# Kernel optimization log

Hardware: AMD Instinct MI355X
Metric: run time of the kernel (lower is better)

## Reference

```python
import jax, jax.numpy as jnp
import numpy as np


def setup_inputs() -> dict:
    key = jax.random.key(0)
    ks = jax.random.split(key, 5)
    B, T, I, H, O = 64, 1024, 128, 256, 128
    stdv = 1.0 / np.sqrt(H)
    return {
        "x": jax.random.normal(ks[0], (B, T, I), dtype=jnp.float32),
        "W": jax.random.uniform(ks[1], (I, 4 * H), dtype=jnp.float32, minval=-stdv, maxval=stdv),
        "U": jax.random.uniform(ks[2], (H, 4 * H), dtype=jnp.float32, minval=-stdv, maxval=stdv),
        "bias": jax.random.uniform(ks[3], (4 * H,), dtype=jnp.float32, minval=-stdv, maxval=stdv),
        "dense_w": jax.random.uniform(ks[4], (O, H), dtype=jnp.float32, minval=-stdv, maxval=stdv),
        "dense_b": jnp.zeros((O,), dtype=jnp.float32),
    }


def reference(x, W, U, bias, dense_w, dense_b):
    B, T, I = x.shape
    H = U.shape[0]
    # Precompute input contribution for all timesteps in one big GEMM.
    xW = jnp.einsum("bti,ig->btg", x, W) + bias  # (B, T, 4H)

    def step(carry, xw_t):
        h, c = carry
        gates = xw_t + h @ U  # (B, 4H)
        i_t = jax.nn.sigmoid(gates[:, :H])
        f_t = jax.nn.sigmoid(gates[:, H:2 * H])
        g_t = jnp.tanh(gates[:, 2 * H:3 * H])
        o_t = jax.nn.sigmoid(gates[:, 3 * H:])
        c = f_t * c + i_t * g_t
        h = o_t * jnp.tanh(c)
        return (h, c), h

    h0 = jnp.zeros((B, H), dtype=x.dtype)
    c0 = jnp.zeros((B, H), dtype=x.dtype)
    (h_T, _), _ = jax.lax.scan(step, (h0, c0), jnp.swapaxes(xW, 0, 1))
    # Original takes hidden_seq[:, -1, :] == final h_t, then Linear, then unsqueeze(2).
    out = h_T @ dense_w.T + dense_b  # (B, O)
    return out[:, :, None]  # (B, O, 1)
```

## Files before the change

kernel.cpp:

```cpp
#include <hip/hip_runtime.h>
#include <math.h>

#define TT 1024
#define BB 64
#define II 128
#define HH 256
#define OO 128
#define GPB 16
#define NCOL 64
#define Z_STRIDE 392
#define PART_BG_STRIDE 68
#define PART_RC_STRIDE 273

#define WS_HBUF_F 8192
#define WS_CLEAR_B 20480

__device__ __forceinline__ float rcp(float v) { return __builtin_amdgcn_rcpf(v); }
__device__ __forceinline__ float sigm(float v) { return rcp(1.f + __expf(-v)); }
__device__ __forceinline__ float ftanh(float v) {
    return __builtin_fmaf(-2.f, rcp(__expf(2.f * v) + 1.f), 1.f);
}

extern "C" __global__ void __launch_bounds__(256, 1) lstm_scan(
    const float* __restrict__ x, const float* __restrict__ W,
    const float* __restrict__ U, const float* __restrict__ bias,
    float* __restrict__ wsf)
{
    __shared__ float z[4 * Z_STRIDE];
    __shared__ float part[16 * PART_RC_STRIDE];
    __shared__ int   misc[8];

    int*   flags  = (int*)wsf;
    int*   abortp = ((int*)wsf) + 4096;
    float* hbuf   = wsf + WS_HBUF_F;

    const int tid  = threadIdx.x;
    const int gid  = blockIdx.x & 15;
    const int p    = blockIdx.x >> 4;
    const int cg   = tid & 15;
    const int rc   = tid >> 4;
    const int lane = tid & 63;
    const int w    = tid >> 6;
    const int myb  = 4 * gid + w;

    float wr[6][4][4];
    {
        const int c0 = cg * 4;
        const int gcol = (c0 >> 4) * HH + p * 16 + (c0 & 15);
#pragma unroll
        for (int rr = 0; rr < 6; ++rr) {
#pragma unroll
            for (int i = 0; i < 4; ++i) {
                const int r = rr * 64 + rc * 4 + i;
                const float4 wv = (rr < 2)
                    ? *(const float4*)(W + (size_t)r * 1024 + gcol)
                    : *(const float4*)(U + (size_t)(r - II) * 1024 + gcol);
                wr[rr][i][0] = wv.x; wr[rr][i][1] = wv.y;
                wr[rr][i][2] = wv.z; wr[rr][i][3] = wv.w;
            }
        }
    }
    const float bia_reg = bias[(lane >> 4) * HH + p * 16 + (lane & 15)];
    float creg = 0.f;

    for (int idx = tid; idx < 4 * Z_STRIDE; idx += 256) z[idx] = 0.f;
    if (tid < 8) misc[tid] = 0;

    if (tid < 128) {
        const int b2 = tid >> 5, l2 = tid & 31;
        const float4 xv = *(const float4*)(
            x + ((size_t)(4 * gid + b2) * TT + 0) * II + 4 * l2);
        *(float4*)(z + b2 * Z_STRIDE + 4 * l2) = xv;
    }
    __syncthreads();

    for (int t = 1; t <= TT; ++t) {
        float acc[4][4];
#pragma unroll
        for (int a = 0; a < 4; ++a)
#pragma unroll
            for (int b = 0; b < 4; ++b) acc[a][b] = 0.f;

#pragma unroll
        for (int rr = 0; rr < 2; ++rr) {
#pragma unroll
            for (int bg = 0; bg < 4; ++bg) {
                const float4 zv = *(const float4*)(z + bg * Z_STRIDE + rr * 64 + rc * 4);
#pragma unroll
                for (int c = 0; c < 4; ++c)
                    acc[bg][c] += zv.x * wr[rr][0][c] + zv.y * wr[rr][1][c]
                                + zv.z * wr[rr][2][c] + zv.w * wr[rr][3][c];
            }
        }

        if (t > 1) {
            const int need = t - 1;
            const int* fp = &flags[((lane & 15) * GPB + gid) * 16 + w * 4];
            int it = 0;
            for (;;) {
                int f1 = need, f2 = need;
                if (lane < GPB) {
                    f1 = __hip_atomic_load(fp, __ATOMIC_RELAXED, __HIP_MEMORY_SCOPE_AGENT);
                    f2 = __hip_atomic_load(fp, __ATOMIC_RELAXED, __HIP_MEMORY_SCOPE_AGENT);
                }
                if (__ballot(f1 >= need) == ~0ULL) break;
                if (__ballot(f2 >= need) == ~0ULL) break;
                if ((++it & 63) == 0) {
                    int abv = __hip_atomic_load(abortp, __ATOMIC_RELAXED,
                                                __HIP_MEMORY_SCOPE_AGENT);
                    if (abv) { if (lane == 0) misc[w] = 1; break; }
                    if (it > (1 << 19)) {
                        if (lane == 0) {
                            __hip_atomic_store(abortp, 1, __ATOMIC_RELAXED,
                                               __HIP_MEMORY_SCOPE_AGENT);
                            misc[w] = 1;
                        }
                        break;
                    }
                }
            }
            const float* hsrc = hbuf + ((size_t)((t - 1) & 1) * BB + myb) * HH;
            const float v0 = __hip_atomic_load(hsrc + lane,       __ATOMIC_RELAXED, __HIP_MEMORY_SCOPE_AGENT);
            const float v1 = __hip_atomic_load(hsrc + lane + 64,  __ATOMIC_RELAXED, __HIP_MEMORY_SCOPE_AGENT);
            const float v2 = __hip_atomic_load(hsrc + lane + 128, __ATOMIC_RELAXED, __HIP_MEMORY_SCOPE_AGENT);
            const float v3 = __hip_atomic_load(hsrc + lane + 192, __ATOMIC_RELAXED, __HIP_MEMORY_SCOPE_AGENT);
            float* zdst = z + w * Z_STRIDE + II + lane;
            zdst[0]   = v0;
            zdst[64]  = v1;
            zdst[128] = v2;
            zdst[192] = v3;
        }
        __syncthreads();
        if (misc[0] | misc[1] | misc[2] | misc[3]) break;

#pragma unroll
        for (int rr = 2; rr < 6; ++rr) {
#pragma unroll
            for (int bg = 0; bg < 4; ++bg) {
                const float4 zv = *(const float4*)(z + bg * Z_STRIDE + rr * 64 + rc * 4);
#pragma unroll
                for (int c = 0; c < 4; ++c)
                    acc[bg][c] += zv.x * wr[rr][0][c] + zv.y * wr[rr][1][c]
                                + zv.z * wr[rr][2][c] + zv.w * wr[rr][3][c];
            }
        }

#pragma unroll
        for (int bg = 0; bg < 4; ++bg)
#pragma unroll
            for (int c = 0; c < 4; ++c)
                part[rc * PART_RC_STRIDE + bg * PART_BG_STRIDE + cg * 4 + c] = acc[bg][c];
        __syncthreads();

        float s = bia_reg;
#pragma unroll
        for (int r2 = 0; r2 < 16; ++r2)
            s += part[r2 * PART_RC_STRIDE + w * PART_BG_STRIDE + lane];

        const int j = lane & 15;
        const float sf = __shfl(s, j + 16);
        const float sg = __shfl(s, j + 32);
        const float so = __shfl(s, j + 48);
        if (lane < 16) {
            const float iv = sigm(s);
            const float fv = sigm(sf);
            const float gv = ftanh(sg);
            const float ov = sigm(so);
            creg = fv * creg + iv * gv;
            const float hv = ov * ftanh(creg);
            __hip_atomic_store(
                hbuf + ((size_t)(t & 1) * BB + myb) * HH + p * 16 + j,
                hv, __ATOMIC_RELAXED, __HIP_MEMORY_SCOPE_AGENT);
        }
        asm volatile("s_waitcnt vmcnt(0)" ::: "memory");
        if (lane == 0)
            __hip_atomic_store(&flags[blockIdx.x * 16 + w * 4], t,
                               __ATOMIC_RELAXED, __HIP_MEMORY_SCOPE_AGENT);

        if (t < TT && lane >= 16 && lane < 48) {
            const int l2 = lane - 16;
            const float4 xv = *(const float4*)(
                x + ((size_t)myb * TT + t) * II + 4 * l2);
            *(float4*)(z + w * Z_STRIDE + 4 * l2) = xv;
        }
        __syncthreads();
    }
}

extern "C" __global__ void __launch_bounds__(256) lstm_out(
    const float* __restrict__ wsf, const float* __restrict__ dw,
    const float* __restrict__ db, float* __restrict__ out)
{
    __shared__ float hs[256];
    __shared__ float red[256];
    const int b = blockIdx.x;
    const int tid = threadIdx.x;
    const float* h0 = wsf + WS_HBUF_F;
    hs[tid] = h0[(size_t)b * HH + tid];
    __syncthreads();
    const int o = tid & 127, half = tid >> 7;
    const float* wrow = dw + o * HH + half * 128;
    const float* hrow = hs + half * 128;
    float s = 0.f;
#pragma unroll
    for (int k = 0; k < 128; k += 4) {
        const float4 wv = *(const float4*)(wrow + k);
        s += hrow[k] * wv.x + hrow[k + 1] * wv.y + hrow[k + 2] * wv.z + hrow[k + 3] * wv.w;
    }
    red[tid] = s;
    __syncthreads();
    if (tid < 128)
        out[(size_t)b * OO + tid] = red[tid] + red[128 + tid] + db[tid];
}

extern "C" void kernel_launch(void* const* d_in, const int* in_sizes, int n_in,
                              void* d_out, int out_size, void* d_ws, size_t ws_size,
                              hipStream_t stream)
{
    const float* x    = (const float*)d_in[0];
    const float* W    = (const float*)d_in[1];
    const float* U    = (const float*)d_in[2];
    const float* bias = (const float*)d_in[3];
    const float* dw   = (const float*)d_in[4];
    const float* db   = (const float*)d_in[5];
    float* out = (float*)d_out;
    float* ws  = (float*)d_ws;

    hipMemsetAsync(d_ws, 0, WS_CLEAR_B, stream);
    hipLaunchKernelGGL(lstm_scan, dim3(256), dim3(256), 0, stream,
                       x, W, U, bias, ws);
    hipLaunchKernelGGL(lstm_out, dim3(64), dim3(256), 0, stream, ws, dw, db, out);
}
```

Before: 2.483 ms.

## Give each wave its own batch row, removing block barriers and LDS reduction

Each wavefront now owns one batch row and computes all 64 of the block's gate columns over the full K=384 reduction, holding 96 float4 weight registers per lane. This removes the cross-thread partial-sum buffer in LDS and every __syncthreads in the time loop, so the waves synchronise only through the global flags. The next timestep's x row is prefetched into registers before the spin-wait. The cost is a 4x longer serial dot product per lane with heavy register pressure (384 weight VGPRs), plus LDS broadcast reads of z.

```diff
diff --git a/kernel.cpp b/kernel.cpp
--- a/kernel.cpp
+++ b/kernel.cpp
@@ -7,10 +7,7 @@
 #define HH 256
 #define OO 128
 #define GPB 16
-#define NCOL 64
-#define Z_STRIDE 392
-#define PART_BG_STRIDE 68
-#define PART_RC_STRIDE 273
+#define ZPAD 400
 
 #define WS_HBUF_F 8192
 #define WS_CLEAR_B 20480
@@ -26,9 +23,7 @@
     const float* __restrict__ U, const float* __restrict__ bias,
     float* __restrict__ wsf)
 {
-    __shared__ float z[4 * Z_STRIDE];
-    __shared__ float part[16 * PART_RC_STRIDE];
-    __shared__ int   misc[8];
+    __shared__ float z[4 * ZPAD];
 
     int*   flags  = (int*)wsf;
     int*   abortp = ((int*)wsf) + 4096;
@@ -37,61 +32,48 @@
     const int tid  = threadIdx.x;
     const int gid  = blockIdx.x & 15;
     const int p    = blockIdx.x >> 4;
-    const int cg   = tid & 15;
-    const int rc   = tid >> 4;
     const int lane = tid & 63;
     const int w    = tid >> 6;
     const int myb  = 4 * gid + w;
+    const int j    = lane & 15;
 
-    float wr[6][4][4];
-    {
-        const int c0 = cg * 4;
-        const int gcol = (c0 >> 4) * HH + p * 16 + (c0 & 15);
+    const int gcol = (lane >> 4) * HH + p * 16 + j;
+
+    float4 wr[96];
 #pragma unroll
-        for (int rr = 0; rr < 6; ++rr) {
-#pragma unroll
-            for (int i = 0; i < 4; ++i) {
-                const int r = rr * 64 + rc * 4 + i;
-                const float4 wv = (rr < 2)
-                    ? *(const float4*)(W + (size_t)r * 1024 + gcol)
-                    : *(const float4*)(U + (size_t)(r - II) * 1024 + gcol);
-                wr[rr][i][0] = wv.x; wr[rr][i][1] = wv.y;
-                wr[rr][i][2] = wv.z; wr[rr][i][3] = wv.w;
-            }
-        }
+    for (int k = 0; k < 96; ++k) {
+        const float* base = (k < 32)
+            ? (W + (size_t)(4 * k) * 1024 + gcol)
+            : (U + (size_t)(4 * k - 128) * 1024 + gcol);
+        wr[k].x = base[0];
+        wr[k].y = base[1024];
+        wr[k].z = base[2048];
+        wr[k].w = base[3072];
     }
-    const float bia_reg = bias[(lane >> 4) * HH + p * 16 + (lane & 15)];
+    const float bia_reg = bias[gcol];
     float creg = 0.f;
 
-    for (int idx = tid; idx < 4 * Z_STRIDE; idx += 256) z[idx] = 0.f;
-    if (tid < 8) misc[tid] = 0;
+    float* zw = z + w * ZPAD;
+    for (int i = lane; i < HH; i += 64) zw[II + i] = 0.f;
+    float4 xv = make_float4(0.f, 0.f, 0.f, 0.f);
+    if (lane < 32) {
+        xv = *(const float4*)(x + (size_t)myb * TT * II + 4 * lane);
+        *(float4*)(zw + 4 * lane) = xv;
+    }
 
-    if (tid < 128) {
-        const int b2 = tid >> 5, l2 = tid & 31;
-        const float4 xv = *(const float4*)(
-            x + ((size_t)(4 * gid + b2) * TT + 0) * II + 4 * l2);
-        *(float4*)(z + b2 * Z_STRIDE + 4 * l2) = xv;
-    }
-    __syncthreads();
-
+    int ab = 0;
     for (int t = 1; t <= TT; ++t) {
-        float acc[4][4];
-#pragma unroll
-        for (int a = 0; a < 4; ++a)
-#pragma unroll
-            for (int b = 0; b < 4; ++b) acc[a][b] = 0.f;
+        float acc[4] = {0.f, 0.f, 0.f, 0.f};
 
 #pragma unroll
-        for (int rr = 0; rr < 2; ++rr) {
-#pragma unroll
-            for (int bg = 0; bg < 4; ++bg) {
-                const float4 zv = *(const float4*)(z + bg * Z_STRIDE + rr * 64 + rc * 4);
-#pragma unroll
-                for (int c = 0; c < 4; ++c)
-                    acc[bg][c] += zv.x * wr[rr][0][c] + zv.y * wr[rr][1][c]
-                                + zv.z * wr[rr][2][c] + zv.w * wr[rr][3][c];
-            }
+        for (int k = 0; k < 32; ++k) {
+            const float4 zv = *(const float4*)(zw + 4 * k);
+            acc[k & 3] += zv.x * wr[k].x + zv.y * wr[k].y
+                        + zv.z * wr[k].z + zv.w * wr[k].w;
         }
+
+        if (t < TT && lane < 32)
+            xv = *(const float4*)(x + ((size_t)myb * TT + t) * II + 4 * lane);
 
         if (t > 1) {
             const int need = t - 1;
@@ -108,56 +90,35 @@
                 if ((++it & 63) == 0) {
                     int abv = __hip_atomic_load(abortp, __ATOMIC_RELAXED,
                                                 __HIP_MEMORY_SCOPE_AGENT);
-                    if (abv) { if (lane == 0) misc[w] = 1; break; }
+                    if (abv) { ab = 1; break; }
                     if (it > (1 << 19)) {
-                        if (lane == 0) {
+                        if (lane == 0)
                             __hip_atomic_store(abortp, 1, __ATOMIC_RELAXED,
                                                __HIP_MEMORY_SCOPE_AGENT);
-                            misc[w] = 1;
-                        }
-                        break;
+                        ab = 1; break;
                     }
                 }
             }
+            if (ab) break;
             const float* hsrc = hbuf + ((size_t)((t - 1) & 1) * BB + myb) * HH;
             const float v0 = __hip_atomic_load(hsrc + lane,       __ATOMIC_RELAXED, __HIP_MEMORY_SCOPE_AGENT);
             const float v1 = __hip_atomic_load(hsrc + lane + 64,  __ATOMIC_RELAXED, __HIP_MEMORY_SCOPE_AGENT);
             const float v2 = __hip_atomic_load(hsrc + lane + 128, __ATOMIC_RELAXED, __HIP_MEMORY_SCOPE_AGENT);
             const float v3 = __hip_atomic_load(hsrc + lane + 192, __ATOMIC_RELAXED, __HIP_MEMORY_SCOPE_AGENT);
-            float* zdst = z + w * Z_STRIDE + II + lane;
-            zdst[0]   = v0;
-            zdst[64]  = v1;
-            zdst[128] = v2;
-            zdst[192] = v3;
-        }
-        __syncthreads();
-        if (misc[0] | misc[1] | misc[2] | misc[3]) break;
-
-#pragma unroll
-        for (int rr = 2; rr < 6; ++rr) {
-#pragma unroll
-            for (int bg = 0; bg < 4; ++bg) {
-                const float4 zv = *(const float4*)(z + bg * Z_STRIDE + rr * 64 + rc * 4);
-#pragma unroll
-                for (int c = 0; c < 4; ++c)
-                    acc[bg][c] += zv.x * wr[rr][0][c] + zv.y * wr[rr][1][c]
-                                + zv.z * wr[rr][2][c] + zv.w * wr[rr][3][c];
-            }
+            zw[II + lane]       = v0;
+            zw[II + lane + 64]  = v1;
+            zw[II + lane + 128] = v2;
+            zw[II + lane + 192] = v3;
         }
 
 #pragma unroll
-        for (int bg = 0; bg < 4; ++bg)
-#pragma unroll
-            for (int c = 0; c < 4; ++c)
-                part[rc * PART_RC_STRIDE + bg * PART_BG_STRIDE + cg * 4 + c] = acc[bg][c];
-        __syncthreads();
+        for (int k = 32; k < 96; ++k) {
+            const float4 zv = *(const float4*)(zw + 4 * k);
+            acc[k & 3] += zv.x * wr[k].x + zv.y * wr[k].y
+                        + zv.z * wr[k].z + zv.w * wr[k].w;
+        }
+        float s = (acc[0] + acc[1]) + (acc[2] + acc[3]) + bia_reg;
 
-        float s = bia_reg;
-#pragma unroll
-        for (int r2 = 0; r2 < 16; ++r2)
-            s += part[r2 * PART_RC_STRIDE + w * PART_BG_STRIDE + lane];
-
-        const int j = lane & 15;
         const float sf = __shfl(s, j + 16);
         const float sg = __shfl(s, j + 32);
         const float so = __shfl(s, j + 48);
@@ -177,13 +138,8 @@
             __hip_atomic_store(&flags[blockIdx.x * 16 + w * 4], t,
                                __ATOMIC_RELAXED, __HIP_MEMORY_SCOPE_AGENT);
 
-        if (t < TT && lane >= 16 && lane < 48) {
-            const int l2 = lane - 16;
-            const float4 xv = *(const float4*)(
-                x + ((size_t)myb * TT + t) * II + 4 * l2);
-            *(float4*)(z + w * Z_STRIDE + 4 * l2) = xv;
-        }
-        __syncthreads();
+        if (t < TT && lane < 32)
+            *(float4*)(zw + 4 * lane) = xv;
     }
 }
 
```

After: 7.350 ms. +196.0%, slower.

## Pack timestep tag with hidden value to replace flag-based cross-block sync

Applied to the files above, without the earlier changes.

Each hidden-state element is now stored as a 64-bit word holding the timestep in the high half and the float in the low half. Consumers poll the h buffer directly until every tag matches the expected step. This removes the separate flag array, the vmcnt wait before the flag store, and the second round of loads after the flag check. Each step trades a flag-then-data round trip for one data poll, at the cost of twice the bytes per h element and polling on the full data.

```diff
diff --git a/kernel.cpp b/kernel.cpp
--- a/kernel.cpp
+++ b/kernel.cpp
@@ -12,8 +12,11 @@
 #define PART_BG_STRIDE 68
 #define PART_RC_STRIDE 273
 
-#define WS_HBUF_F 8192
-#define WS_CLEAR_B 20480
+#define WS_HBUF_B 16384
+#define WS_CLEAR_B (WS_HBUF_B + 2 * BB * HH * 8)
+
+typedef unsigned long long u64;
+typedef unsigned int u32;
 
 __device__ __forceinline__ float rcp(float v) { return __builtin_amdgcn_rcpf(v); }
 __device__ __forceinline__ float sigm(float v) { return rcp(1.f + __expf(-v)); }
@@ -30,9 +33,8 @@
     __shared__ float part[16 * PART_RC_STRIDE];
     __shared__ int   misc[8];
 
-    int*   flags  = (int*)wsf;
-    int*   abortp = ((int*)wsf) + 4096;
-    float* hbuf   = wsf + WS_HBUF_F;
+    int* abortp = (int*)wsf;
+    u64* hbuf   = (u64*)((char*)wsf + WS_HBUF_B);
 
     const int tid  = threadIdx.x;
     const int gid  = blockIdx.x & 15;
@@ -42,6 +44,7 @@
     const int lane = tid & 63;
     const int w    = tid >> 6;
     const int myb  = 4 * gid + w;
+    const int j    = lane & 15;
 
     float wr[6][4][4];
     {
@@ -60,7 +63,7 @@
             }
         }
     }
-    const float bia_reg = bias[(lane >> 4) * HH + p * 16 + (lane & 15)];
+    const float bia_reg = bias[(lane >> 4) * HH + p * 16 + j];
     float creg = 0.f;
 
     for (int idx = tid; idx < 4 * Z_STRIDE; idx += 256) z[idx] = 0.f;
@@ -94,41 +97,36 @@
         }
 
         if (t > 1) {
-            const int need = t - 1;
-            const int* fp = &flags[((lane & 15) * GPB + gid) * 16 + w * 4];
-            int it = 0;
+            const u32 want = (u32)(t - 1);
+            const u64* hsrc = hbuf + ((size_t)((t - 1) & 1) * BB + myb) * HH;
+            u64 n0, n1, n2, n3;
+            int it = 0, ab = 0;
             for (;;) {
-                int f1 = need, f2 = need;
-                if (lane < GPB) {
-                    f1 = __hip_atomic_load(fp, __ATOMIC_RELAXED, __HIP_MEMORY_SCOPE_AGENT);
-                    f2 = __hip_atomic_load(fp, __ATOMIC_RELAXED, __HIP_MEMORY_SCOPE_AGENT);
-                }
-                if (__ballot(f1 >= need) == ~0ULL) break;
-                if (__ballot(f2 >= need) == ~0ULL) break;
+                n0 = __hip_atomic_load(hsrc + lane,       __ATOMIC_RELAXED, __HIP_MEMORY_SCOPE_AGENT);
+                n1 = __hip_atomic_load(hsrc + lane + 64,  __ATOMIC_RELAXED, __HIP_MEMORY_SCOPE_AGENT);
+                n2 = __hip_atomic_load(hsrc + lane + 128, __ATOMIC_RELAXED, __HIP_MEMORY_SCOPE_AGENT);
+                n3 = __hip_atomic_load(hsrc + lane + 192, __ATOMIC_RELAXED, __HIP_MEMORY_SCOPE_AGENT);
+                const bool ok = ((u32)(n0 >> 32) == want) && ((u32)(n1 >> 32) == want)
+                             && ((u32)(n2 >> 32) == want) && ((u32)(n3 >> 32) == want);
+                if (__ballot(ok) == ~0ULL) break;
                 if ((++it & 63) == 0) {
                     int abv = __hip_atomic_load(abortp, __ATOMIC_RELAXED,
                                                 __HIP_MEMORY_SCOPE_AGENT);
-                    if (abv) { if (lane == 0) misc[w] = 1; break; }
+                    if (abv) { ab = 1; break; }
                     if (it > (1 << 19)) {
-                        if (lane == 0) {
+                        if (lane == 0)
                             __hip_atomic_store(abortp, 1, __ATOMIC_RELAXED,
                                                __HIP_MEMORY_SCOPE_AGENT);
-                            misc[w] = 1;
-                        }
-                        break;
+                        ab = 1; break;
                     }
                 }
             }
-            const float* hsrc = hbuf + ((size_t)((t - 1) & 1) * BB + myb) * HH;
-            const float v0 = __hip_atomic_load(hsrc + lane,       __ATOMIC_RELAXED, __HIP_MEMORY_SCOPE_AGENT);
-            const float v1 = __hip_atomic_load(hsrc + lane + 64,  __ATOMIC_RELAXED, __HIP_MEMORY_SCOPE_AGENT);
-            const float v2 = __hip_atomic_load(hsrc + lane + 128, __ATOMIC_RELAXED, __HIP_MEMORY_SCOPE_AGENT);
-            const float v3 = __hip_atomic_load(hsrc + lane + 192, __ATOMIC_RELAXED, __HIP_MEMORY_SCOPE_AGENT);
+            if (ab && lane == 0) misc[w] = 1;
             float* zdst = z + w * Z_STRIDE + II + lane;
-            zdst[0]   = v0;
-            zdst[64]  = v1;
-            zdst[128] = v2;
-            zdst[192] = v3;
+            zdst[0]   = __uint_as_float((u32)n0);
+            zdst[64]  = __uint_as_float((u32)n1);
+            zdst[128] = __uint_as_float((u32)n2);
+            zdst[192] = __uint_as_float((u32)n3);
         }
         __syncthreads();
         if (misc[0] | misc[1] | misc[2] | misc[3]) break;
@@ -157,7 +155,6 @@
         for (int r2 = 0; r2 < 16; ++r2)
             s += part[r2 * PART_RC_STRIDE + w * PART_BG_STRIDE + lane];
 
-        const int j = lane & 15;
         const float sf = __shfl(s, j + 16);
         const float sg = __shfl(s, j + 32);
         const float so = __shfl(s, j + 48);
@@ -168,16 +165,11 @@
             const float ov = sigm(so);
             creg = fv * creg + iv * gv;
             const float hv = ov * ftanh(creg);
+            const u64 pk = ((u64)(u32)t << 32) | (u64)__float_as_uint(hv);
             __hip_atomic_store(
                 hbuf + ((size_t)(t & 1) * BB + myb) * HH + p * 16 + j,
-                hv, __ATOMIC_RELAXED, __HIP_MEMORY_SCOPE_AGENT);
-        }
-        asm volatile("s_waitcnt vmcnt(0)" ::: "memory");
-        if (lane == 0)
-            __hip_atomic_store(&flags[blockIdx.x * 16 + w * 4], t,
-                               __ATOMIC_RELAXED, __HIP_MEMORY_SCOPE_AGENT);
-
-        if (t < TT && lane >= 16 && lane < 48) {
+                pk, __ATOMIC_RELAXED, __HIP_MEMORY_SCOPE_AGENT);
+        } else if (lane < 48 && t < TT) {
             const int l2 = lane - 16;
             const float4 xv = *(const float4*)(
                 x + ((size_t)myb * TT + t) * II + 4 * l2);
@@ -195,8 +187,8 @@
     __shared__ float red[256];
     const int b = blockIdx.x;
     const int tid = threadIdx.x;
-    const float* h0 = wsf + WS_HBUF_F;
-    hs[tid] = h0[(size_t)b * HH + tid];
+    const u64* h0 = (const u64*)((const char*)wsf + WS_HBUF_B);
+    hs[tid] = __uint_as_float((u32)h0[(size_t)b * HH + tid]);
     __syncthreads();
     const int o = tid & 127, half = tid >> 7;
     const float* wrow = dw + o * HH + half * 128;
```

Result: faster. 2.113 ms (median of 2 runs) (-14.9%).
